# Kernel tuning notes

Hardware: AMD Instinct MI355X
Metric: run time of the kernel (lower is better)

The kernel has to match this reference:

```python
import jax, jax.numpy as jnp
import numpy as np

B = 32          # graphs per batch
NPG = 512       # nodes per graph
EPG = 2048      # original edges per graph (stored in y[:, -1])
N = B * NPG     # 16384 nodes
E = B * EPG     # 65536 edges
GF = 5          # num_global_features
ETOT = E + N    # edges after add_self_loops

def _lin(k, o, i):
    return jax.random.normal(k, (o, i), jnp.float32) / np.sqrt(i)

def setup_inputs():
    key = jax.random.key(0)
    ks = jax.random.split(key, 20)
    x = jax.random.normal(ks[0], (N,), jnp.float32)
    off = (jnp.arange(B, dtype=jnp.int32) * NPG)[:, None]
    src = (jax.random.randint(ks[1], (B, EPG), 0, NPG, dtype=jnp.int32) + off).reshape(-1)
    dst = (jax.random.randint(ks[2], (B, EPG), 0, NPG, dtype=jnp.int32) + off).reshape(-1)
    edge_index = jnp.stack([src, dst])
    edge_attr = jax.random.normal(ks[3], (E, GF), jnp.float32)
    # last global feature = number of edges per graph (module reads y[:, -1])
    y = jax.random.normal(ks[4], (B, GF), jnp.float32).at[:, -1].set(float(EPG)).reshape(-1)
    batch_vector = jnp.repeat(jnp.arange(B, dtype=jnp.int32), NPG)
    p = dict(
        Wn=_lin(ks[5], 512, 1), bn=jnp.zeros(512, jnp.float32),
        We=_lin(ks[6], 511, GF), be=jnp.zeros(511, jnp.float32),
        Wg=_lin(ks[7], 512, GF), bg=jnp.zeros(512, jnp.float32),
        Wl=_lin(ks[8], 1024, 512), bl=jnp.zeros(1024, jnp.float32),
        Wr=_lin(ks[9], 1024, 512), br=jnp.zeros(1024, jnp.float32),
        Wge=_lin(ks[10], 1024, 511),
        att=jax.random.normal(ks[11], (1024,), jnp.float32) / 32.0,
        bgat=jnp.zeros(1024, jnp.float32),
        Wm=_lin(ks[12], 1024, 1024), bm=jnp.zeros(1024, jnp.float32),
        Wmi=_lin(ks[13], 1024, 1024), bmi=jnp.zeros(1024, jnp.float32),
        Wce=_lin(ks[14], 1024, 512), bce=jnp.zeros(1024, jnp.float32),
        W1=_lin(ks[15], 256, 2048), b1=jnp.zeros(256, jnp.float32),
        W2=_lin(ks[16], 1, 256), b2=jnp.zeros(1, jnp.float32),
    )
    return dict(x=x, edge_index=edge_index, edge_attr=edge_attr, y=y,
                batch_vector=batch_vector, **p)

def _leaky(v, s=0.01):
    return jnp.where(v >= 0, v, s * v)

def _forward(edge_index, batch_vector, x, edge_attr, y, Wn, bn, We, be, Wg, bg,
             Wl, bl, Wr, br, Wge, att, bgat, Wm, bm, Wmi, bmi, Wce, bce,
             W1, b1, W2, b2):
    # add_self_loops (fill_value=1.0 for edge_attr), self loops appended last
    loops = jnp.arange(N, dtype=edge_index.dtype)
    src = jnp.concatenate([edge_index[0], loops])
    dst = jnp.concatenate([edge_index[1], loops])
    ea = jnp.concatenate([edge_attr, jnp.ones((N, GF), edge_attr.dtype)], axis=0)
    # preprocessing MLPs (dropout = identity at inference)
    h = _leaky(x[:, None] @ Wn.T + bn)               # [N, 512]
    e = _leaky(ea @ We.T + be)                       # [ETOT, 511]
    yg = _leaky(y.reshape(B, GF) @ Wg.T + bg)        # [B, 512]
    # GATv2Conv, 1 head, concat, negative_slope=0.2, no self-loop add
    xl = h @ Wl.T + bl                               # source transform [N, 1024]
    xr = h @ Wr.T + br                               # target transform [N, 1024]
    m = _leaky(xl[src] + xr[dst] + e @ Wge.T, 0.2)   # [ETOT, 1024]
    logit = m @ att                                  # [ETOT]
    mx = jax.ops.segment_max(logit, dst, num_segments=N)
    ex = jnp.exp(logit - mx[dst])
    alpha = ex / (jax.ops.segment_sum(ex, dst, num_segments=N)[dst] + 1e-16)
    gat = jax.ops.segment_sum(alpha[:, None] * xl[src], dst, num_segments=N) + bgat
    edge_total = jnp.concatenate([e, alpha[:, None]], axis=1)  # [ETOT, 512]
    # GeneralConv: undirected message, add aggregation, identity skip (in==out)
    hm = gat @ Wm.T + bm
    hmi = gat @ Wmi.T + bmi
    eh = edge_total @ Wce.T + bce                    # [ETOT, 1024]
    deg = jax.ops.segment_sum(jnp.ones((ETOT,), gat.dtype), dst, num_segments=N)
    conv = (jax.ops.segment_sum(hm[src] + eh, dst, num_segments=N)
            + deg[:, None] * hmi + gat)              # [N, 1024]
    # global mean pooling (nodes) and module's contiguous edge batch vector
    nc = jax.ops.segment_sum(jnp.ones((N,), conv.dtype), batch_vector, num_segments=B)
    pn = jax.ops.segment_sum(conv, batch_vector, num_segments=B) / nc[:, None]
    ebatch = jnp.repeat(jnp.arange(B, dtype=jnp.int32), EPG + NPG)
    pe = jax.ops.segment_sum(edge_total, ebatch, num_segments=B) / float(EPG + NPG)
    pooled = jnp.concatenate([pn, pe, yg], axis=1)   # [B, 2048]
    out = _leaky(pooled @ W1.T + b1) @ W2.T + b2
    return jax.nn.sigmoid(out)                       # [B, 1]

def reference(x, edge_index, edge_attr, y, batch_vector, Wn, bn, We, be, Wg, bg,
              Wl, bl, Wr, br, Wge, att, bgat, Wm, bm, Wmi, bmi, Wce, bce,
              W1, b1, W2, b2):
    return _forward(edge_index, batch_vector, x, edge_attr, y, Wn, bn, We, be,
                    Wg, bg, Wl, bl, Wr, br, Wge, att, bgat, Wm, bm, Wmi, bmi,
                    Wce, bce, W1, b1, W2, b2)
```

## Files before the change

kernel.cpp:

```cpp
#include <hip/hip_runtime.h>
#include <cstdint>
#include <cstddef>

#define N_NODES 16384
#define N_EDGES 65536
#define ETOT    81920
#define B_GR    32

typedef __attribute__((ext_vector_type(8))) short bf16x8;
typedef __attribute__((ext_vector_type(4))) float f32x4;

static constexpr size_t OFF_XL    = 0;
static constexpr size_t OFF_XR    = 33554432ULL;
static constexpr size_t OFF_EBF   = 67108864ULL;
static constexpr size_t OFF_HBF   = 67108864ULL;
static constexpr size_t OFF_WCAT  = 83886080ULL;
static constexpr size_t OFF_ROWP  = 67108864ULL;
static constexpr size_t OFF_CSR   = 67174656ULL;
static constexpr size_t OFF_ALPHA = 67502336ULL;
static constexpr size_t OFF_WGEP  = 134217728ULL;
static constexpr size_t OFF_LPART = 135266304ULL;
static constexpr size_t OFF_DEG   = 137363456ULL;
static constexpr size_t OFF_ODEG  = 137428992ULL;
static constexpr size_t OFF_CURS  = 137494528ULL;
static constexpr size_t OFF_PG    = 137560064ULL;
static constexpr size_t OFF_PDG   = 137691136ULL;
static constexpr size_t OFF_PGAT  = 137822208ULL;
static constexpr size_t OFF_PS    = 137953280ULL;
static constexpr size_t OFF_PE    = 138018816ULL;
static constexpr size_t OFF_WLOOP = 138084352ULL;
static constexpr size_t OFF_YG    = 138088448ULL;
static constexpr size_t OFF_PN    = 138153984ULL;

__device__ __forceinline__ float leaky01(float v){ return v >= 0.f ? v : 0.01f*v; }
__device__ __forceinline__ float leaky02(float v){ return v >= 0.f ? v : 0.2f*v; }
__device__ __forceinline__ unsigned short f2bf(float f){
  union { float f; unsigned u; } v; v.f = f;
  unsigned r = v.u + 0x7FFFu + ((v.u >> 16) & 1u);
  return (unsigned short)(r >> 16);
}
__device__ __forceinline__ float bf2f(unsigned short h){
  union { unsigned u; float f; } v; v.u = ((unsigned)h) << 16;
  return v.f;
}

__global__ __launch_bounds__(256) void k_prep0(
    const float* __restrict__ x, const float* __restrict__ Wn, const float* __restrict__ bn,
    const float* __restrict__ Wl, const float* __restrict__ Wr,
    const float* __restrict__ Wge, const float* __restrict__ y,
    const float* __restrict__ Wg, const float* __restrict__ bg,
    const float* __restrict__ We, const float* __restrict__ be,
    float* __restrict__ zone, unsigned short* __restrict__ h_bf,
    unsigned short* __restrict__ Wcat, unsigned short* __restrict__ Wge_p,
    float* __restrict__ yg, float* __restrict__ we_loop) {
  __shared__ float e_lds[512];
  int bx = blockIdx.x, tid = threadIdx.x;
  if (bx < 176) {
    ((float4*)zone)[bx*256 + tid] = (float4){0.f,0.f,0.f,0.f};
  } else if (bx < 1200) {
    int gid = (bx-176)*256 + tid;
    int base = gid*8;
    int n = base >> 9, j = base & 511;
    float xv = x[n];
    float4 w0 = *(const float4*)(Wn + j);
    float4 w1 = *(const float4*)(Wn + j + 4);
    float4 b0 = *(const float4*)(bn + j);
    float4 b1 = *(const float4*)(bn + j + 4);
    unsigned short o[8];
    o[0]=f2bf(leaky01(xv*w0.x+b0.x)); o[1]=f2bf(leaky01(xv*w0.y+b0.y));
    o[2]=f2bf(leaky01(xv*w0.z+b0.z)); o[3]=f2bf(leaky01(xv*w0.w+b0.w));
    o[4]=f2bf(leaky01(xv*w1.x+b1.x)); o[5]=f2bf(leaky01(xv*w1.y+b1.y));
    o[6]=f2bf(leaky01(xv*w1.z+b1.z)); o[7]=f2bf(leaky01(xv*w1.w+b1.w));
    ((uint4*)h_bf)[gid] = *(const uint4*)o;
  } else if (bx < 2224) {
    int i = (bx-1200)*256 + tid;
    int base = i*4;
    const float* src = (base < 524288) ? (Wl + base) : (Wr + base - 524288);
    float4 v = *(const float4*)src;
    ushort4 o; o.x=f2bf(v.x); o.y=f2bf(v.y); o.z=f2bf(v.z); o.w=f2bf(v.w);
    ((ushort4*)Wcat)[i] = o;
  } else if (bx < 4272) {
    int gid = (bx-2224)*256 + tid;
    int j = gid >> 9, k = gid & 511;
    Wge_p[gid] = (k < 511) ? f2bf(Wge[(size_t)j*511 + k]) : (unsigned short)0;
  } else if (bx < 4336) {
    int gid = (bx-4272)*256 + tid;
    int b = gid >> 9, j = gid & 511;
    float s = bg[j];
    #pragma unroll
    for (int k=0;k<5;k++) s += y[b*5+k]*Wg[j*5+k];
    yg[gid] = leaky01(s);
  } else {
    for (int c = tid; c < 512; c += 256) {
      float v = 0.f;
      if (c < 511) {
        float s = be[c];
        #pragma unroll
        for (int q=0;q<5;q++) s += We[c*5+q];
        v = leaky01(s);
      }
      e_lds[c] = v;
    }
    __syncthreads();
    int j = (bx-4336)*256 + tid;
    float s = 0.f;
    for (int k=0;k<511;k++) s += e_lds[k]*Wge[(size_t)j*511+k];
    we_loop[j] = s;
  }
}

__global__ __launch_bounds__(256) void k_prep_e(
    const float* __restrict__ ea, const float* __restrict__ We, const float* __restrict__ be,
    unsigned short* __restrict__ E_bf) {
  int gid = blockIdx.x*256 + threadIdx.x;
  int e = gid >> 6, cg = gid & 63;
  int c0 = cg*8;
  const float* e5 = ea + (size_t)e*5;
  float a0=e5[0], a1=e5[1], a2=e5[2], a3=e5[3], a4=e5[4];
  unsigned short o[8];
  #pragma unroll
  for (int j=0;j<8;j++) {
    int c = c0 + j;
    float v = 0.f;
    if (c < 511) {
      const float* w = We + c*5;
      float s = be[c] + a0*w[0] + a1*w[1] + a2*w[2] + a3*w[3] + a4*w[4];
      v = leaky01(s);
    }
    o[j] = f2bf(v);
  }
  ((uint4*)E_bf)[gid] = *(const uint4*)o;
}

__global__ void k_deg(const int* __restrict__ ei, int* __restrict__ deg, int* __restrict__ odeg) {
  int i = blockIdx.x*blockDim.x + threadIdx.x;
  int s, d;
  if (i < N_EDGES) { s = ei[i]; d = ei[N_EDGES + i]; }
  else { s = i - N_EDGES; d = s; }
  atomicAdd(&deg[d], 1);
  atomicAdd(&odeg[s], 1);
}

__global__ __launch_bounds__(1024) void k_scan(const int* __restrict__ deg, int* __restrict__ rowptr) {
  __shared__ int sums[1024];
  int t = threadIdx.x;
  int local[16]; int s = 0;
  #pragma unroll
  for (int i=0;i<16;i++){ local[i] = deg[t*16+i]; s += local[i]; }
  sums[t] = s; __syncthreads();
  for (int off=1; off<1024; off<<=1) {
    int v = (t >= off) ? sums[t-off] : 0;
    __syncthreads();
    sums[t] += v;
    __syncthreads();
  }
  int run = (t==0) ? 0 : sums[t-1];
  if (t==0) rowptr[0] = 0;
  #pragma unroll
  for (int i=0;i<16;i++){ run += local[i]; rowptr[t*16+i+1] = run; }
}

__global__ void k_fill_csr(const int* __restrict__ ei, const int* __restrict__ rowptr,
                           int* __restrict__ cursor, int* __restrict__ csr) {
  int i = blockIdx.x*blockDim.x + threadIdx.x;
  int d = (i < N_EDGES) ? ei[N_EDGES + i] : (i - N_EDGES);
  int pos = rowptr[d] + atomicAdd(&cursor[d], 1);
  csr[pos] = i;
}


__global__ __launch_bounds__(256) void k_gemm_xlxr(
    const unsigned short* __restrict__ h_bf, const unsigned short* __restrict__ Wcat,
    const float* __restrict__ bl, const float* __restrict__ br,
    unsigned short* __restrict__ xl_bf, unsigned short* __restrict__ xr_bf) {
  __shared__ unsigned short As[2][4096];
  __shared__ unsigned short Bs[2][4096];
  int blk = blockIdx.x;
  int xcd = blk & 7, slot = blk >> 3;
  int bx = xcd*16 + (slot >> 4), by = slot & 15;
  int row0 = bx*128, col0 = by*128;
  int tid = threadIdx.x;
  int w = tid >> 6, lane = tid & 63;
  int wm = w >> 1, wn = w & 1;
  int quad = lane >> 4, l16 = lane & 15;
  int ldoff = w*512 + lane*8;
  const unsigned short* gA = h_bf + (size_t)(row0 + w*16 + l16)*512 + quad*8;
  const unsigned short* gB = Wcat + (size_t)(col0 + w*16 + l16)*512 + quad*8;
  f32x4 acc[4][4];
  #pragma unroll
  for (int i=0;i<4;i++)
    #pragma unroll
    for (int j=0;j<4;j++) acc[i][j] = (f32x4){0.f,0.f,0.f,0.f};

  {
    uint4 a0 = *(const uint4*)(gA);
    uint4 a1 = *(const uint4*)(gA + 32768);
    uint4 b0 = *(const uint4*)(gB);
    uint4 b1 = *(const uint4*)(gB + 32768);
    *(uint4*)&As[0][ldoff] = a0; *(uint4*)&As[0][2048+ldoff] = a1;
    *(uint4*)&Bs[0][ldoff] = b0; *(uint4*)&Bs[0][2048+ldoff] = b1;
  }
  __syncthreads();
  int cur = 0;
  #pragma unroll 2
  for (int k0 = 32; k0 <= 512; k0 += 32) {
    uint4 na0, na1, nb0, nb1;
    bool more = (k0 < 512);
    if (more) {
      na0 = *(const uint4*)(gA + k0);
      na1 = *(const uint4*)(gA + 32768 + k0);
      nb0 = *(const uint4*)(gB + k0);
      nb1 = *(const uint4*)(gB + 32768 + k0);
    }
    bf16x8 af[4], bfr[4];
    #pragma unroll
    for (int mi=0;mi<4;mi++)
      af[mi] = *(const bf16x8*)&As[cur][(wm*4+mi)*512 + quad*128 + l16*8];
    #pragma unroll
    for (int ni=0;ni<4;ni++)
      bfr[ni] = *(const bf16x8*)&Bs[cur][(wn*4+ni)*512 + quad*128 + l16*8];
    #pragma unroll
    for (int mi=0;mi<4;mi++)
      #pragma unroll
      for (int ni=0;ni<4;ni++)
        acc[mi][ni] = __builtin_amdgcn_mfma_f32_16x16x32_bf16(af[mi], bfr[ni], acc[mi][ni], 0, 0, 0);
    if (more) {
      *(uint4*)&As[cur^1][ldoff] = na0; *(uint4*)&As[cur^1][2048+ldoff] = na1;
      *(uint4*)&Bs[cur^1][ldoff] = nb0; *(uint4*)&Bs[cur^1][2048+ldoff] = nb1;
    }
    __syncthreads();
    cur ^= 1;
  }
  bool isL = (by < 8);
  const float* bias = isL ? bl : br;
  unsigned short* O = isL ? xl_bf : xr_bf;
  int cb = isL ? col0 : (col0 - 1024);
  float bias4[4];
  #pragma unroll
  for (int ni=0;ni<4;ni++) bias4[ni] = bias[cb + wn*64 + ni*16 + l16];
  #pragma unroll
  for (int mi=0;mi<4;mi++)
    #pragma unroll
    for (int ni=0;ni<4;ni++) {
      int col = cb + wn*64 + ni*16 + l16;
      #pragma unroll
      for (int r=0;r<4;r++) {
        int row = row0 + wm*64 + mi*16 + quad*4 + r;
        O[(size_t)row*1024 + col] = f2bf(acc[mi][ni][r] + bias4[ni]);
      }
    }
}

__global__ __launch_bounds__(256) void k_mfma_we(
    const unsigned short* __restrict__ E_bf, const unsigned short* __restrict__ Wge_bf,
    const int* __restrict__ ei,
    const unsigned short* __restrict__ xl_bf, const unsigned short* __restrict__ xr_bf,
    const float* __restrict__ att, float* __restrict__ logit_part) {
  __shared__ unsigned short As[2][4096];
  __shared__ unsigned short Bs[2][4096];
  __shared__ float tmp[128];
  int blk = blockIdx.x;
  int xcd = blk & 7, slot = blk >> 3;
  int bx = xcd*64 + (slot >> 3), by = slot & 7;
  int row0 = bx*128, col0 = by*128;
  int tid = threadIdx.x;
  int w = tid >> 6, lane = tid & 63;
  int wm = w >> 1, wn = w & 1;
  int quad = lane >> 4, l16 = lane & 15;
  int ldoff = w*512 + lane*8;
  const unsigned short* gA = E_bf  + (size_t)(row0 + w*16 + l16)*512 + quad*8;
  const unsigned short* gB = Wge_bf + (size_t)(col0 + w*16 + l16)*512 + quad*8;
  f32x4 acc[4][4];
  #pragma unroll
  for (int i=0;i<4;i++)
    #pragma unroll
    for (int j=0;j<4;j++) acc[i][j] = (f32x4){0.f,0.f,0.f,0.f};

  {
    uint4 a0 = *(const uint4*)(gA);
    uint4 a1 = *(const uint4*)(gA + 32768);
    uint4 b0 = *(const uint4*)(gB);
    uint4 b1 = *(const uint4*)(gB + 32768);
    *(uint4*)&As[0][ldoff] = a0; *(uint4*)&As[0][2048+ldoff] = a1;
    *(uint4*)&Bs[0][ldoff] = b0; *(uint4*)&Bs[0][2048+ldoff] = b1;
  }
  __syncthreads();
  int cur = 0;
  #pragma unroll 2
  for (int k0 = 32; k0 <= 512; k0 += 32) {
    uint4 na0, na1, nb0, nb1;
    bool more = (k0 < 512);
    if (more) {
      na0 = *(const uint4*)(gA + k0);
      na1 = *(const uint4*)(gA + 32768 + k0);
      nb0 = *(const uint4*)(gB + k0);
      nb1 = *(const uint4*)(gB + 32768 + k0);
    }
    bf16x8 af[4], bfr[4];
    #pragma unroll
    for (int mi=0;mi<4;mi++)
      af[mi] = *(const bf16x8*)&As[cur][(wm*4+mi)*512 + quad*128 + l16*8];
    #pragma unroll
    for (int ni=0;ni<4;ni++)
      bfr[ni] = *(const bf16x8*)&Bs[cur][(wn*4+ni)*512 + quad*128 + l16*8];
    #pragma unroll
    for (int mi=0;mi<4;mi++)
      #pragma unroll
      for (int ni=0;ni<4;ni++)
        acc[mi][ni] = __builtin_amdgcn_mfma_f32_16x16x32_bf16(af[mi], bfr[ni], acc[mi][ni], 0, 0, 0);
    if (more) {
      *(uint4*)&As[cur^1][ldoff] = na0; *(uint4*)&As[cur^1][2048+ldoff] = na1;
      *(uint4*)&Bs[cur^1][ldoff] = nb0; *(uint4*)&Bs[cur^1][2048+ldoff] = nb1;
    }
    __syncthreads();
    cur ^= 1;
  }
  float att4[4];
  #pragma unroll
  for (int ni=0;ni<4;ni++) att4[ni] = att[col0 + wn*64 + ni*16 + l16];
  float pv[4][4];
  #pragma unroll
  for (int mi=0;mi<4;mi++) {
    #pragma unroll
    for (int r=0;r<4;r++) {
      int e = row0 + wm*64 + mi*16 + quad*4 + r;
      int s = ei[e], d = ei[N_EDGES + e];
      const unsigned short* xlr = xl_bf + (size_t)s*1024;
      const unsigned short* xrr = xr_bf + (size_t)d*1024;
      float p = 0.f;
      #pragma unroll
      for (int ni=0;ni<4;ni++) {
        int col = col0 + wn*64 + ni*16 + l16;
        float z = acc[mi][ni][r] + bf2f(xlr[col]) + bf2f(xrr[col]);
        z = leaky02(z);
        p += z*att4[ni];
      }
      p += __shfl_down(p, 8, 16);
      p += __shfl_down(p, 4, 16);
      p += __shfl_down(p, 2, 16);
      p += __shfl_down(p, 1, 16);
      pv[mi][r] = p;
    }
  }
  if (wn == 1 && l16 == 0) {
    #pragma unroll
    for (int mi=0;mi<4;mi++)
      #pragma unroll
      for (int r=0;r<4;r++)
        tmp[wm*64 + mi*16 + quad*4 + r] = pv[mi][r];
  }
  __syncthreads();
  if (wn == 0 && l16 == 0) {
    #pragma unroll
    for (int mi=0;mi<4;mi++)
      #pragma unroll
      for (int r=0;r<4;r++) {
        int le = wm*64 + mi*16 + quad*4 + r;
        logit_part[(size_t)(row0 + le)*8 + by] = pv[mi][r] + tmp[le];
      }
  }
}

__global__ __launch_bounds__(256) void k_softmax_gat(
    const int* __restrict__ ei, const int* __restrict__ rowptr, const int* __restrict__ csr,
    const float* __restrict__ logit_part,
    const unsigned short* __restrict__ xl_bf, const unsigned short* __restrict__ xr_bf,
    const float* __restrict__ we_loop, const float* __restrict__ att,
    const float* __restrict__ bgat,
    float* __restrict__ alpha, unsigned short* __restrict__ gat_bf) {
  __shared__ float sl[256];
  __shared__ int   se[256];
  __shared__ float red[256];
  int blk = blockIdx.x;
  int n = ((blk & 7) << 11) + (blk >> 3);
  int tid = threadIdx.x;
  {
    ushort4 a = ((const ushort4*)(xl_bf + (size_t)n*1024))[tid];
    ushort4 b = ((const ushort4*)(xr_bf + (size_t)n*1024))[tid];
    float4 c = ((const float4*)we_loop)[tid];
    float4 t = ((const float4*)att)[tid];
    float s = 0.f;
    s += leaky02(bf2f(a.x)+bf2f(b.x)+c.x)*t.x;
    s += leaky02(bf2f(a.y)+bf2f(b.y)+c.y)*t.y;
    s += leaky02(bf2f(a.z)+bf2f(b.z)+c.z)*t.z;
    s += leaky02(bf2f(a.w)+bf2f(b.w)+c.w)*t.w;
    red[tid] = s;
  }
  __syncthreads();
  #pragma unroll
  for (int off=128; off; off>>=1){ if (tid<off) red[tid] += red[tid+off]; __syncthreads(); }
  float sll = red[0];
  __syncthreads();

  int beg = rowptr[n], end = rowptr[n+1], cnt = end - beg;
  float m = -1e30f;
  for (int p = beg+tid; p < end; p += 256) {
    int e = csr[p];
    float lg;
    if (e < N_EDGES) {
      const float4* lp = (const float4*)(logit_part + (size_t)e*8);
      float4 q0 = lp[0], q1 = lp[1];
      lg = q0.x+q0.y+q0.z+q0.w+q1.x+q1.y+q1.z+q1.w;
    } else lg = sll;
    int idx = p - beg;
    if (idx < 256) { se[idx] = e; sl[idx] = lg; }
    m = fmaxf(m, lg);
  }
  red[tid] = m; __syncthreads();
  #pragma unroll
  for (int off=128; off; off>>=1){ if (tid<off) red[tid] = fmaxf(red[tid], red[tid+off]); __syncthreads(); }
  m = red[0];
  __syncthreads();
  float ss = 0.f;
  for (int p = beg+tid; p < end; p += 256) {
    int idx = p - beg;
    ss += expf(sl[idx] - m);
  }
  red[tid] = ss; __syncthreads();
  #pragma unroll
  for (int off=128; off; off>>=1){ if (tid<off) red[tid] += red[tid+off]; __syncthreads(); }
  float inv = 1.f/(red[0] + 1e-16f);
  __syncthreads();
  for (int p = beg+tid; p < end; p += 256) {
    int idx = p - beg;
    float a = expf(sl[idx] - m)*inv;
    alpha[se[idx]] = a;
    sl[idx] = a;
  }
  __syncthreads();
  float4 acc = ((const float4*)bgat)[tid];
  for (int p = 0; p < cnt; p++) {
    float a = sl[p]; int e = se[p];
    int s = (e < N_EDGES) ? ei[e] : (e - N_EDGES);
    ushort4 v = ((const ushort4*)(xl_bf + (size_t)s*1024))[tid];
    acc.x += a*bf2f(v.x); acc.y += a*bf2f(v.y); acc.z += a*bf2f(v.z); acc.w += a*bf2f(v.w);
  }
  ushort4 o; o.x=f2bf(acc.x); o.y=f2bf(acc.y); o.z=f2bf(acc.z); o.w=f2bf(acc.w);
  ((ushort4*)(gat_bf + (size_t)n*1024))[tid] = o;
}

__global__ __launch_bounds__(256) void k_nodepool(
    const unsigned short* __restrict__ gat_bf, const int* __restrict__ odeg,
    const int* __restrict__ rowptr,
    float* __restrict__ P_G, float* __restrict__ P_DG, float* __restrict__ P_gat) {
  int b = blockIdx.x, yy = blockIdx.y;
  int nc = yy >> 2, cg = yy & 3;
  int col = cg*256 + threadIdx.x;
  float a1=0.f, a2=0.f, a3=0.f;
  int n0 = b*512 + nc*128;
  for (int i=0;i<128;i++){
    int n = n0 + i;
    float g = bf2f(gat_bf[(size_t)n*1024 + col]);
    float od = (float)odeg[n];
    float dg = (float)(rowptr[n+1]-rowptr[n]);
    a1 += od*g; a2 += dg*g; a3 += g;
  }
  atomicAdd(&P_G[b*1024+col], a1);
  atomicAdd(&P_DG[b*1024+col], a2);
  atomicAdd(&P_gat[b*1024+col], a3);
}

__global__ __launch_bounds__(256) void k_edgepool(
    const float* __restrict__ ea, const float* __restrict__ We, const float* __restrict__ be,
    const float* __restrict__ alpha, float* __restrict__ P_S, float* __restrict__ pe) {
  __shared__ float sea[640];
  __shared__ float sal[128];
  int b = blockIdx.x, chy = blockIdx.y, tid = threadIdx.x;
  int mode = (chy < 20) ? 0 : 1;
  int ch = (chy < 20) ? chy : (chy - 20);
  int c1 = tid, c2 = tid + 256;
  bool v2 = (c2 < 511);
  float w1[5], w2[5]={0,0,0,0,0}, b1v, b2v=0.f;
  #pragma unroll
  for (int q=0;q<5;q++) w1[q] = We[c1*5+q];
  b1v = be[c1];
  if (v2) {
    #pragma unroll
    for (int q=0;q<5;q++) w2[q] = We[c2*5+q];
    b2v = be[c2];
  }
  int base = (mode == 0)
    ? ((ch < 16) ? (b*2048 + ch*128) : (N_EDGES + b*512 + (ch-16)*128))
    : (b*2560 + ch*128);
  for (int i=tid;i<640;i+=256){
    int r = base + i/5;
    sea[i] = (r < N_EDGES) ? ea[(size_t)r*5 + (i%5)] : 1.0f;
  }
  for (int i=tid;i<128;i+=256) sal[i] = alpha[base + i];
  __syncthreads();
  float acc1 = 0.f, acc2 = 0.f;
  for (int rr=0; rr<128; rr++) {
    const float* er = &sea[rr*5];
    acc1 += leaky01(b1v + er[0]*w1[0]+er[1]*w1[1]+er[2]*w1[2]+er[3]*w1[3]+er[4]*w1[4]);
    if (v2) acc2 += leaky01(b2v + er[0]*w2[0]+er[1]*w2[1]+er[2]*w2[2]+er[3]*w2[3]+er[4]*w2[4]);
    else    acc2 += sal[rr];
  }
  if (mode == 0) {
    atomicAdd(&P_S[b*512+c1], acc1);
    atomicAdd(&P_S[b*512+c2], acc2);
  } else {
    const float sc = 1.f/2560.f;
    atomicAdd(&pe[b*512+c1], acc1*sc);
    atomicAdd(&pe[b*512+c2], acc2*sc);
  }
}

__global__ __launch_bounds__(256) void k_pn(
    const float* __restrict__ P_G, const float* __restrict__ P_DG,
    const float* __restrict__ P_S, const float* __restrict__ P_gat,
    const float* __restrict__ Wm, const float* __restrict__ bm,
    const float* __restrict__ Wmi, const float* __restrict__ bmi,
    const float* __restrict__ Wce, const float* __restrict__ bce,
    float* __restrict__ pn) {
  __shared__ float sPg[1024], sPdg[1024], sPs[512];
  int b = blockIdx.x, col0 = blockIdx.y*64;
  int tid = threadIdx.x, w = tid >> 6, lane = tid & 63;
  for (int i=tid;i<1024;i+=256){ sPg[i]=P_G[b*1024+i]; sPdg[i]=P_DG[b*1024+i]; }
  for (int i=tid;i<512;i+=256) sPs[i]=P_S[b*512+i];
  __syncthreads();
  for (int c=0;c<16;c++){
    int j = col0 + w*16 + c;
    const float* wm  = Wm  + (size_t)j*1024;
    const float* wmi = Wmi + (size_t)j*1024;
    const float* wce = Wce + (size_t)j*512;
    float s = 0.f;
    #pragma unroll 4
    for (int i=0;i<16;i++){ int k = lane + i*64; s += sPg[k]*wm[k] + sPdg[k]*wmi[k]; }
    #pragma unroll 4
    for (int i=0;i<8;i++){ int k = lane + i*64; s += sPs[k]*wce[k]; }
    #pragma unroll
    for (int off=32; off; off>>=1) s += __shfl_down(s, off);
    if (lane == 0) {
      pn[b*1024+j] = (s + P_gat[b*1024+j] + 2560.f*(bm[j]+bmi[j]+bce[j])) * (1.f/512.f);
    }
  }
}

__global__ __launch_bounds__(256) void k_final(
    const float* __restrict__ pn, const float* __restrict__ pe, const float* __restrict__ yg,
    const float* __restrict__ W1, const float* __restrict__ b1,
    const float* __restrict__ W2, const float* __restrict__ b2,
    float* __restrict__ out) {
  __shared__ float pooled[2048];
  __shared__ float red[256];
  int b = blockIdx.x, tid = threadIdx.x;
  for (int i=tid;i<1024;i+=256) pooled[i]      = pn[b*1024+i];
  for (int i=tid;i<512;i+=256)  pooled[1024+i] = pe[b*512+i];
  for (int i=tid;i<512;i+=256)  pooled[1536+i] = yg[b*512+i];
  __syncthreads();
  const float4* w4 = (const float4*)(W1 + (size_t)tid*2048);
  const float4* p4 = (const float4*)pooled;
  float s = b1[tid];
  for (int k=0;k<512;k++){
    float4 w = w4[k]; float4 p = p4[k];
    s += w.x*p.x + w.y*p.y + w.z*p.z + w.w*p.w;
  }
  s = leaky01(s);
  red[tid] = s * W2[tid];
  __syncthreads();
  for (int off=128; off; off>>=1){
    if (tid < off) red[tid] += red[tid+off];
    __syncthreads();
  }
  if (tid == 0){
    float o = red[0] + b2[0];
    out[b] = 1.f/(1.f+expf(-o));
  }
}

extern "C" void kernel_launch(void* const* d_in, const int* in_sizes, int n_in,
                              void* d_out, int out_size, void* d_ws, size_t ws_size,
                              hipStream_t stream) {
  const float* x   = (const float*)d_in[0];
  const int*   ei  = (const int*)  d_in[1];
  const float* ea  = (const float*)d_in[2];
  const float* y   = (const float*)d_in[3];
  const float* Wn  = (const float*)d_in[5];
  const float* bn  = (const float*)d_in[6];
  const float* We  = (const float*)d_in[7];
  const float* be  = (const float*)d_in[8];
  const float* Wg  = (const float*)d_in[9];
  const float* bg  = (const float*)d_in[10];
  const float* Wl  = (const float*)d_in[11];
  const float* bl  = (const float*)d_in[12];
  const float* Wr  = (const float*)d_in[13];
  const float* br  = (const float*)d_in[14];
  const float* Wge = (const float*)d_in[15];
  const float* att = (const float*)d_in[16];
  const float* bgat= (const float*)d_in[17];
  const float* Wm  = (const float*)d_in[18];
  const float* bm  = (const float*)d_in[19];
  const float* Wmi = (const float*)d_in[20];
  const float* bmi = (const float*)d_in[21];
  const float* Wce = (const float*)d_in[22];
  const float* bce = (const float*)d_in[23];
  const float* W1  = (const float*)d_in[24];
  const float* b1  = (const float*)d_in[25];
  const float* W2  = (const float*)d_in[26];
  const float* b2  = (const float*)d_in[27];
  float* out = (float*)d_out;

  char* ws = (char*)d_ws;
  unsigned short* xl_bf  = (unsigned short*)(ws + OFF_XL);
  unsigned short* xr_bf  = (unsigned short*)(ws + OFF_XR);
  unsigned short* gat_bf = (unsigned short*)(ws + OFF_XR);
  unsigned short* E_bf   = (unsigned short*)(ws + OFF_EBF);
  unsigned short* h_bf   = (unsigned short*)(ws + OFF_HBF);
  unsigned short* Wcat   = (unsigned short*)(ws + OFF_WCAT);
  unsigned short* Wge_p  = (unsigned short*)(ws + OFF_WGEP);
  float* lpart  = (float*)(ws + OFF_LPART);
  float* zone   = (float*)(ws + OFF_DEG);
  int*   deg    = (int*)  (ws + OFF_DEG);
  int*   odeg   = (int*)  (ws + OFF_ODEG);
  int*   cursor = (int*)  (ws + OFF_CURS);
  float* P_G    = (float*)(ws + OFF_PG);
  float* P_DG   = (float*)(ws + OFF_PDG);
  float* P_gat  = (float*)(ws + OFF_PGAT);
  float* P_S    = (float*)(ws + OFF_PS);
  float* pe     = (float*)(ws + OFF_PE);
  int*   rowptr = (int*)  (ws + OFF_ROWP);
  int*   csr    = (int*)  (ws + OFF_CSR);
  float* alpha  = (float*)(ws + OFF_ALPHA);
  float* we_loop= (float*)(ws + OFF_WLOOP);
  float* yg     = (float*)(ws + OFF_YG);
  float* pn     = (float*)(ws + OFF_PN);

  k_prep0<<<dim3(4340), dim3(256), 0, stream>>>(x, Wn, bn, Wl, Wr, Wge, y, Wg, bg, We, be,
                                                zone, h_bf, Wcat, Wge_p, yg, we_loop);
  k_gemm_xlxr<<<dim3(2048), dim3(256), 0, stream>>>(h_bf, Wcat, bl, br, xl_bf, xr_bf);
  k_prep_e<<<dim3(16384), dim3(256), 0, stream>>>(ea, We, be, E_bf);
  k_mfma_we<<<dim3(4096), dim3(256), 0, stream>>>(E_bf, Wge_p, ei, xl_bf, xr_bf, att, lpart);
  k_deg<<<dim3(320), dim3(256), 0, stream>>>(ei, deg, odeg);
  k_scan<<<dim3(1), dim3(1024), 0, stream>>>(deg, rowptr);
  k_fill_csr<<<dim3(320), dim3(256), 0, stream>>>(ei, rowptr, cursor, csr);
  k_softmax_gat<<<dim3(16384), dim3(256), 0, stream>>>(ei, rowptr, csr, lpart, xl_bf, xr_bf,
                                                       we_loop, att, bgat, alpha, gat_bf);
  k_nodepool<<<dim3(32,16), dim3(256), 0, stream>>>(gat_bf, odeg, rowptr, P_G, P_DG, P_gat);
  k_edgepool<<<dim3(32,40), dim3(256), 0, stream>>>(ea, We, be, alpha, P_S, pe);
  k_pn<<<dim3(32,16), dim3(256), 0, stream>>>(P_G, P_DG, P_S, P_gat, Wm, bm, Wmi, bmi, Wce, bce, pn);
  k_final<<<dim3(32), dim3(256), 0, stream>>>(pn, pe, yg, W1, b1, W2, b2, out);
}
```

Measured before the change: 617.2 us.

## Fuse degree count into edge prep, vectorize node pooling, XCD-aware pn block mapping

Folds the degree-counting kernel into the edge-feature prep kernel as extra blocks, which removes one launch. The node pooling kernel now has each thread load four bf16 columns with one vector load and uses 4x fewer blocks. The pn kernel moves to a 1D grid whose block index is remapped so that blocks sharing a column group of Wm/Wmi/Wce land on the same XCD, aiming at better L2 reuse of the weights. The trade-off is less parallelism in nodepool and more register pressure from the per-thread accumulators.

```diff
diff --git a/kernel.cpp b/kernel.cpp
--- a/kernel.cpp
+++ b/kernel.cpp
@@ -111,34 +111,36 @@
 
 __global__ __launch_bounds__(256) void k_prep_e(
     const float* __restrict__ ea, const float* __restrict__ We, const float* __restrict__ be,
-    unsigned short* __restrict__ E_bf) {
-  int gid = blockIdx.x*256 + threadIdx.x;
-  int e = gid >> 6, cg = gid & 63;
-  int c0 = cg*8;
-  const float* e5 = ea + (size_t)e*5;
-  float a0=e5[0], a1=e5[1], a2=e5[2], a3=e5[3], a4=e5[4];
-  unsigned short o[8];
-  #pragma unroll
-  for (int j=0;j<8;j++) {
-    int c = c0 + j;
-    float v = 0.f;
-    if (c < 511) {
-      const float* w = We + c*5;
-      float s = be[c] + a0*w[0] + a1*w[1] + a2*w[2] + a3*w[3] + a4*w[4];
-      v = leaky01(s);
-    }
-    o[j] = f2bf(v);
-  }
-  ((uint4*)E_bf)[gid] = *(const uint4*)o;
-}
-
-__global__ void k_deg(const int* __restrict__ ei, int* __restrict__ deg, int* __restrict__ odeg) {
-  int i = blockIdx.x*blockDim.x + threadIdx.x;
-  int s, d;
-  if (i < N_EDGES) { s = ei[i]; d = ei[N_EDGES + i]; }
-  else { s = i - N_EDGES; d = s; }
-  atomicAdd(&deg[d], 1);
-  atomicAdd(&odeg[s], 1);
+    unsigned short* __restrict__ E_bf,
+    const int* __restrict__ ei, int* __restrict__ deg, int* __restrict__ odeg) {
+  int blk = blockIdx.x;
+  if (blk < 16384) {
+    int gid = blk*256 + threadIdx.x;
+    int e = gid >> 6, cg = gid & 63;
+    int c0 = cg*8;
+    const float* e5 = ea + (size_t)e*5;
+    float a0=e5[0], a1=e5[1], a2=e5[2], a3=e5[3], a4=e5[4];
+    unsigned short o[8];
+    #pragma unroll
+    for (int j=0;j<8;j++) {
+      int c = c0 + j;
+      float v = 0.f;
+      if (c < 511) {
+        const float* w = We + c*5;
+        float s = be[c] + a0*w[0] + a1*w[1] + a2*w[2] + a3*w[3] + a4*w[4];
+        v = leaky01(s);
+      }
+      o[j] = f2bf(v);
+    }
+    ((uint4*)E_bf)[gid] = *(const uint4*)o;
+  } else {
+    int i = (blk-16384)*256 + threadIdx.x;
+    int s, d;
+    if (i < N_EDGES) { s = ei[i]; d = ei[N_EDGES + i]; }
+    else { s = i - N_EDGES; d = s; }
+    atomicAdd(&deg[d], 1);
+    atomicAdd(&odeg[s], 1);
+  }
 }
 
 __global__ __launch_bounds__(1024) void k_scan(const int* __restrict__ deg, int* __restrict__ rowptr) {
@@ -443,21 +445,26 @@
     const unsigned short* __restrict__ gat_bf, const int* __restrict__ odeg,
     const int* __restrict__ rowptr,
     float* __restrict__ P_G, float* __restrict__ P_DG, float* __restrict__ P_gat) {
-  int b = blockIdx.x, yy = blockIdx.y;
-  int nc = yy >> 2, cg = yy & 3;
-  int col = cg*256 + threadIdx.x;
-  float a1=0.f, a2=0.f, a3=0.f;
+  int b = blockIdx.x, nc = blockIdx.y;
+  int c4 = threadIdx.x;
+  float a1[4]={0,0,0,0}, a2[4]={0,0,0,0}, a3[4]={0,0,0,0};
   int n0 = b*512 + nc*128;
   for (int i=0;i<128;i++){
     int n = n0 + i;
-    float g = bf2f(gat_bf[(size_t)n*1024 + col]);
+    ushort4 g4 = ((const ushort4*)(gat_bf + (size_t)n*1024))[c4];
     float od = (float)odeg[n];
     float dg = (float)(rowptr[n+1]-rowptr[n]);
-    a1 += od*g; a2 += dg*g; a3 += g;
-  }
-  atomicAdd(&P_G[b*1024+col], a1);
-  atomicAdd(&P_DG[b*1024+col], a2);
-  atomicAdd(&P_gat[b*1024+col], a3);
+    float g0 = bf2f(g4.x), g1 = bf2f(g4.y), g2 = bf2f(g4.z), g3 = bf2f(g4.w);
+    a1[0]+=od*g0; a1[1]+=od*g1; a1[2]+=od*g2; a1[3]+=od*g3;
+    a2[0]+=dg*g0; a2[1]+=dg*g1; a2[2]+=dg*g2; a2[3]+=dg*g3;
+    a3[0]+=g0; a3[1]+=g1; a3[2]+=g2; a3[3]+=g3;
+  }
+  #pragma unroll
+  for (int j=0;j<4;j++){
+    atomicAdd(&P_G [b*1024 + c4*4+j], a1[j]);
+    atomicAdd(&P_DG[b*1024 + c4*4+j], a2[j]);
+    atomicAdd(&P_gat[b*1024 + c4*4+j], a3[j]);
+  }
 }
 
 __global__ __launch_bounds__(256) void k_edgepool(
@@ -513,7 +520,11 @@
     const float* __restrict__ Wce, const float* __restrict__ bce,
     float* __restrict__ pn) {
   __shared__ float sPg[1024], sPdg[1024], sPs[512];
-  int b = blockIdx.x, col0 = blockIdx.y*64;
+  int blk = blockIdx.x;
+  int xcd = blk & 7, slot = blk >> 3;
+  int colgrp = xcd*2 + (slot & 1);
+  int b = slot >> 1;
+  int col0 = colgrp*64;
   int tid = threadIdx.x, w = tid >> 6, lane = tid & 63;
   for (int i=tid;i<1024;i+=256){ sPg[i]=P_G[b*1024+i]; sPdg[i]=P_DG[b*1024+i]; }
   for (int i=tid;i<512;i+=256) sPs[i]=P_S[b*512+i];
@@ -628,15 +639,14 @@
   k_prep0<<<dim3(4340), dim3(256), 0, stream>>>(x, Wn, bn, Wl, Wr, Wge, y, Wg, bg, We, be,
                                                 zone, h_bf, Wcat, Wge_p, yg, we_loop);
   k_gemm_xlxr<<<dim3(2048), dim3(256), 0, stream>>>(h_bf, Wcat, bl, br, xl_bf, xr_bf);
-  k_prep_e<<<dim3(16384), dim3(256), 0, stream>>>(ea, We, be, E_bf);
+  k_prep_e<<<dim3(16704), dim3(256), 0, stream>>>(ea, We, be, E_bf, ei, deg, odeg);
   k_mfma_we<<<dim3(4096), dim3(256), 0, stream>>>(E_bf, Wge_p, ei, xl_bf, xr_bf, att, lpart);
-  k_deg<<<dim3(320), dim3(256), 0, stream>>>(ei, deg, odeg);
   k_scan<<<dim3(1), dim3(1024), 0, stream>>>(deg, rowptr);
   k_fill_csr<<<dim3(320), dim3(256), 0, stream>>>(ei, rowptr, cursor, csr);
   k_softmax_gat<<<dim3(16384), dim3(256), 0, stream>>>(ei, rowptr, csr, lpart, xl_bf, xr_bf,
                                                        we_loop, att, bgat, alpha, gat_bf);
-  k_nodepool<<<dim3(32,16), dim3(256), 0, stream>>>(gat_bf, odeg, rowptr, P_G, P_DG, P_gat);
+  k_nodepool<<<dim3(32,4), dim3(256), 0, stream>>>(gat_bf, odeg, rowptr, P_G, P_DG, P_gat);
   k_edgepool<<<dim3(32,40), dim3(256), 0, stream>>>(ea, We, be, alpha, P_S, pe);
-  k_pn<<<dim3(32,16), dim3(256), 0, stream>>>(P_G, P_DG, P_S, P_gat, Wm, bm, Wmi, bmi, Wce, bce, pn);
+  k_pn<<<dim3(512), dim3(256), 0, stream>>>(P_G, P_DG, P_S, P_gat, Wm, bm, Wmi, bmi, Wce, bce, pn);
   k_final<<<dim3(32), dim3(256), 0, stream>>>(pn, pe, yg, W1, b1, W2, b2, out);
 }
```

New measurement: 631.4 us. +2.3%, slower.
